# Optimization experiments

Measured on AMD Instinct MI355X. Metric: run time of the kernel, lower is better.

## Reference

```python
import jax, jax.numpy as jnp
import numpy as np

DIM = 768
D_STATE = 16
D_INNER = 2 * DIM  # expand=2


def setup_inputs() -> dict:
    key = jax.random.key(0)
    k_x, k_in, k_conv, k_out = jax.random.split(key, 4)
    B, L = 1, 4096
    x = jax.random.normal(k_x, (B, L, DIM), dtype=jnp.float32)
    # torch Linear weight layout: [out_features, in_features]
    W_in = jax.random.normal(k_in, (3 * D_INNER + 2 * D_STATE, DIM), dtype=jnp.float32) * 0.02
    # depthwise conv1d kernel: [out_ch=d_inner, in_ch/groups=1, k=3]
    W_conv = jax.random.normal(k_conv, (D_INNER, 1, 3), dtype=jnp.float32) * 0.1
    W_out = jax.random.normal(k_out, (DIM, D_INNER), dtype=jnp.float32) * 0.02
    A_log = jnp.log(jnp.tile(jnp.arange(1, D_STATE + 1, dtype=jnp.float32), (D_INNER, 1)))
    D = jnp.ones((D_INNER,), dtype=jnp.float32)
    return {"x": x, "W_in": W_in, "W_conv": W_conv, "W_out": W_out, "A_log": A_log, "D": D}


def reference(x, W_in, W_conv, W_out, A_log, D):
    d_inner = W_conv.shape[0]
    d_state = A_log.shape[1]
    Bsz = x.shape[0]

    xz = x @ W_in.T  # [B, L, 3*d_inner + 2*d_state]
    x_inner, z, B_ssm, C_ssm, delta = jnp.split(
        xz, [d_inner, 2 * d_inner, 2 * d_inner + d_state, 2 * d_inner + 2 * d_state], axis=-1
    )

    # depthwise conv over sequence: [B, d_inner, L]
    xc = jax.lax.conv_general_dilated(
        x_inner.transpose(0, 2, 1), W_conv,
        window_strides=(1,), padding=[(1, 1)], feature_group_count=d_inner,
    ).transpose(0, 2, 1)  # back to [B, L, d_inner]
    xc = jax.nn.silu(xc)

    A = -jnp.exp(A_log)  # [d_inner, d_state]
    delta = jax.nn.softplus(delta)  # [B, L, d_inner]
    dA = jnp.exp(jnp.einsum('bld,dn->bldn', delta, A))           # [B, L, d_inner, d_state]
    dBx = jnp.einsum('bld,bln,bld->bldn', delta, B_ssm, xc)      # delta_B * x fused

    def step(h, inp):
        da_t, dbx_t, c_t = inp  # [B,d,n], [B,d,n], [B,n]
        h = da_t * h + dbx_t
        y_t = jnp.einsum('bdn,bn->bd', h, c_t)
        return h, y_t

    h0 = jnp.zeros((Bsz, d_inner, d_state), dtype=x.dtype)
    _, ys = jax.lax.scan(
        step, h0,
        (dA.transpose(1, 0, 2, 3), dBx.transpose(1, 0, 2, 3), C_ssm.transpose(1, 0, 2)),
    )  # ys: [L, B, d_inner]

    y = ys.transpose(1, 0, 2) + xc * D  # skip connection
    y = y * jax.nn.silu(z)
    return y @ W_out.T  # [B, L, dim]
```

## Files before the change

kernel.cpp:

```cpp
#include <hip/hip_runtime.h>
#include <hip/hip_bf16.h>
#include <math.h>

#define LSEQ   4096
#define DIM    768
#define DINNER 1536
#define DSTATE 16
#define NCOLS  4640
#define NCH    256
#define CLEN   16
#define NPAD   4736
#define DXW    1568

typedef _Float16 f16;
typedef __attribute__((ext_vector_type(2))) _Float16 f16x2;
typedef __attribute__((ext_vector_type(4))) _Float16 f16x4;
typedef __attribute__((ext_vector_type(8))) _Float16 f16x8;
typedef __attribute__((ext_vector_type(4))) float f32x4;

__device__ __forceinline__ void gld_lds16(void* lds_dst, const void* gsrc) {
    __builtin_amdgcn_global_load_lds(
        (__attribute__((address_space(1))) void*)(gsrc),
        (__attribute__((address_space(3))) void*)(lds_dst), 16, 0, 0);
}

#define G1K    768
#define G1_NT  12
#define G1_BM  256
#define G1_BN  128
#define G1_RT  384
#define G1_LDSE (G1_RT * 64)

__global__ __launch_bounds__(512) void gemm1_pipe(const f16* __restrict__ A,
                                                  const f16* __restrict__ B,
                                                  float* __restrict__ C,
                                                  f16* __restrict__ Xb,
                                                  f16* __restrict__ Zb) {
    __shared__ __align__(16) f16 S[3 * G1_LDSE];

    const int P   = gridDim.x >> 3;
    const int idx = (blockIdx.x & 7) * P + (blockIdx.x >> 3);
    const int sm  = idx / 296;
    const int rem = idx - sm * 296;
    const int m0  = (sm * 8 + (rem & 7)) * G1_BM;
    const int n0  = (rem >> 3) * G1_BN;

    const int tid  = threadIdx.x;
    const int w    = tid >> 6;
    const int lane = tid & 63;
    const int wr   = w >> 1;
    const int wc   = w & 1;
    const int m    = lane & 15;
    const int q    = lane >> 4;
    const int rl8  = lane >> 3;
    const int bsel = lane & 7;

    const f16* gb[6];
#pragma unroll
    for (int s = 0; s < 6; ++s) {
        const int rl  = (w + 8 * s) * 8 + rl8;
        const int blk = bsel ^ (rl & 7);
        gb[s] = (rl < G1_BM) ? A + (size_t)(m0 + rl) * G1K + blk * 8
                             : B + (size_t)(n0 + rl - G1_BM) * G1K + blk * 8;
    }

    f32x4 acc[4][4];
#pragma unroll
    for (int i = 0; i < 4; i++)
#pragma unroll
        for (int j = 0; j < 4; j++) acc[i][j] = (f32x4){0.f, 0.f, 0.f, 0.f};

    auto stg2 = [&](int kt, int s0) {
        f16* dst = S + (kt % 3) * G1_LDSE;
#pragma unroll
        for (int s = s0; s < s0 + 2; ++s)
            gld_lds16(dst + (w + 8 * s) * 512, gb[s] + kt * 64);
    };
    auto stg6 = [&](int kt) {
        f16* dst = S + (kt % 3) * G1_LDSE;
#pragma unroll
        for (int s = 0; s < 6; ++s)
            gld_lds16(dst + (w + 8 * s) * 512, gb[s] + kt * 64);
    };

    stg6(0);
    stg6(1);

#pragma unroll
    for (int kt = 0; kt < G1_NT; ++kt) {
        if (kt < G1_NT - 1) asm volatile("s_waitcnt vmcnt(6)" ::: "memory");
        else                asm volatile("s_waitcnt vmcnt(0)" ::: "memory");
        __builtin_amdgcn_s_barrier();
        const f16* As = S + (kt % 3) * G1_LDSE;
        const f16* Bs = As + G1_BM * 64;
        const bool pf = (kt + 2 < G1_NT);

        f16x8 af0[2][2], af2[2][2], bh0[2][2], bh2[2][2];

#pragma unroll
        for (int kk = 0; kk < 2; ++kk) {
            const int fo = (((q + 4 * kk) ^ (m & 7)) << 3);
#pragma unroll
            for (int i = 0; i < 2; ++i) {
                af0[kk][i] = *(const f16x8*)&As[(wr * 64 + i * 16 + m) * 64 + fo];
                bh0[kk][i] = *(const f16x8*)&Bs[(wc * 64 + i * 16 + m) * 64 + fo];
            }
        }
        if (pf) stg2(kt + 2, 0);
        __builtin_amdgcn_s_barrier();
        asm volatile("s_waitcnt lgkmcnt(0)" ::: "memory");
        __builtin_amdgcn_sched_barrier(0);
        __builtin_amdgcn_s_setprio(1);
#pragma unroll
        for (int kk = 0; kk < 2; ++kk)
#pragma unroll
            for (int i = 0; i < 2; ++i)
#pragma unroll
                for (int j = 0; j < 2; ++j)
                    acc[i][j] = __builtin_amdgcn_mfma_f32_16x16x32_f16(
                        af0[kk][i], bh0[kk][j], acc[i][j], 0, 0, 0);
        __builtin_amdgcn_s_setprio(0);

#pragma unroll
        for (int kk = 0; kk < 2; ++kk) {
            const int fo = (((q + 4 * kk) ^ (m & 7)) << 3);
#pragma unroll
            for (int j = 0; j < 2; ++j)
                bh2[kk][j] = *(const f16x8*)&Bs[(wc * 64 + (j + 2) * 16 + m) * 64 + fo];
        }
        if (pf) stg2(kt + 2, 2);
        __builtin_amdgcn_s_barrier();
        asm volatile("s_waitcnt lgkmcnt(0)" ::: "memory");
        __builtin_amdgcn_sched_barrier(0);
        __builtin_amdgcn_s_setprio(1);
#pragma unroll
        for (int kk = 0; kk < 2; ++kk)
#pragma unroll
            for (int i = 0; i < 2; ++i)
#pragma unroll
                for (int j = 0; j < 2; ++j)
                    acc[i][j + 2] = __builtin_amdgcn_mfma_f32_16x16x32_f16(
                        af0[kk][i], bh2[kk][j], acc[i][j + 2], 0, 0, 0);
        __builtin_amdgcn_s_setprio(0);

#pragma unroll
        for (int kk = 0; kk < 2; ++kk) {
            const int fo = (((q + 4 * kk) ^ (m & 7)) << 3);
#pragma unroll
            for (int i = 0; i < 2; ++i)
                af2[kk][i] = *(const f16x8*)&As[(wr * 64 + (i + 2) * 16 + m) * 64 + fo];
        }
        if (pf) stg2(kt + 2, 4);
        __builtin_amdgcn_s_barrier();
        asm volatile("s_waitcnt lgkmcnt(0)" ::: "memory");
        __builtin_amdgcn_sched_barrier(0);
        __builtin_amdgcn_s_setprio(1);
#pragma unroll
        for (int kk = 0; kk < 2; ++kk)
#pragma unroll
            for (int i = 0; i < 2; ++i)
#pragma unroll
                for (int j = 0; j < 2; ++j)
                    acc[i + 2][j] = __builtin_amdgcn_mfma_f32_16x16x32_f16(
                        af2[kk][i], bh0[kk][j], acc[i + 2][j], 0, 0, 0);
        __builtin_amdgcn_s_setprio(0);

        __builtin_amdgcn_s_setprio(1);
#pragma unroll
        for (int kk = 0; kk < 2; ++kk)
#pragma unroll
            for (int i = 0; i < 2; ++i)
#pragma unroll
                for (int j = 0; j < 2; ++j)
                    acc[i + 2][j + 2] = __builtin_amdgcn_mfma_f32_16x16x32_f16(
                        af2[kk][i], bh2[kk][j], acc[i + 2][j + 2], 0, 0, 0);
        __builtin_amdgcn_s_setprio(0);
    }

    if (n0 < DINNER) {
#pragma unroll
        for (int i = 0; i < 4; i++)
#pragma unroll
            for (int j = 0; j < 4; j++) {
                const int col  = n0 + wc * 64 + j * 16 + m;
                const int rowb = m0 + wr * 64 + i * 16 + q * 4;
#pragma unroll
                for (int r = 0; r < 4; r++)
                    Xb[(size_t)(rowb + r) * DINNER + col] = (f16)acc[i][j][r];
            }
        return;
    }
    if (n0 < 2 * DINNER) {
#pragma unroll
        for (int i = 0; i < 4; i++)
#pragma unroll
            for (int j = 0; j < 4; j++) {
                const int col  = n0 - DINNER + wc * 64 + j * 16 + m;
                const int rowb = m0 + wr * 64 + i * 16 + q * 4;
#pragma unroll
                for (int r = 0; r < 4; r++)
                    Zb[(size_t)(rowb + r) * DINNER + col] = (f16)acc[i][j][r];
            }
        return;
    }
#pragma unroll
    for (int i = 0; i < 4; i++)
#pragma unroll
        for (int j = 0; j < 4; j++) {
            const int col = n0 - 2 * DINNER + wc * 64 + j * 16 + m;
            if (col >= DXW) continue;
            const int rowb = m0 + wr * 64 + i * 16 + q * 4;
#pragma unroll
            for (int r = 0; r < 4; r++)
                C[(size_t)(rowb + r) * DXW + col] = acc[i][j][r];
        }
}

#define G2K    1536
#define G2_NT  24
#define G2_LDSE (128 * 64)

__global__ __launch_bounds__(256) void gemm2_pipe(const f16* __restrict__ A,
                                                  const f16* __restrict__ B,
                                                  float* __restrict__ C) {
    __shared__ __align__(16) f16 S[3 * G2_LDSE];

    const int P   = gridDim.x >> 3;
    const int idx = (blockIdx.x & 7) * P + (blockIdx.x >> 3);
    const int m0  = (idx / 12) * 64;
    const int n0  = (idx % 12) * 64;

    const int tid  = threadIdx.x;
    const int w    = tid >> 6;
    const int lane = tid & 63;
    const int wr   = w >> 1;
    const int wc   = w & 1;
    const int m    = lane & 15;
    const int q    = lane >> 4;
    const int rl8  = lane >> 3;
    const int bsel = lane & 7;

    const f16* gb[4];
#pragma unroll
    for (int s = 0; s < 4; ++s) {
        const int rl  = (w + 4 * s) * 8 + rl8;
        const int blk = bsel ^ (rl & 7);
        gb[s] = (rl < 64) ? A + (size_t)(m0 + rl) * G2K + blk * 8
                          : B + (size_t)(n0 + rl - 64) * G2K + blk * 8;
    }

    f32x4 acc[2][2];
#pragma unroll
    for (int i = 0; i < 2; i++)
#pragma unroll
        for (int j = 0; j < 2; j++) acc[i][j] = (f32x4){0.f, 0.f, 0.f, 0.f};

    auto stg = [&](int kt) {
        f16* dst = S + (kt % 3) * G2_LDSE;
#pragma unroll
        for (int s = 0; s < 4; ++s)
            gld_lds16(dst + (w + 4 * s) * 512, gb[s] + kt * 64);
    };

    stg(0);
    stg(1);

#pragma unroll
    for (int kt = 0; kt < G2_NT; ++kt) {
        if (kt < G2_NT - 1) asm volatile("s_waitcnt vmcnt(4)" ::: "memory");
        else                asm volatile("s_waitcnt vmcnt(0)" ::: "memory");
        __builtin_amdgcn_s_barrier();
        if (kt + 2 < G2_NT) stg(kt + 2);

        const f16* As = S + (kt % 3) * G2_LDSE;
        const f16* Bs = As + 64 * 64;

        f16x8 af[2][2], bh[2][2];
#pragma unroll
        for (int kk = 0; kk < 2; ++kk) {
            const int fo = (((q + 4 * kk) ^ (m & 7)) << 3);
#pragma unroll
            for (int i = 0; i < 2; ++i) {
                af[kk][i] = *(const f16x8*)&As[(wr * 32 + i * 16 + m) * 64 + fo];
                bh[kk][i] = *(const f16x8*)&Bs[(wc * 32 + i * 16 + m) * 64 + fo];
            }
        }
        asm volatile("s_waitcnt lgkmcnt(0)" ::: "memory");
        __builtin_amdgcn_sched_barrier(0);
        __builtin_amdgcn_s_setprio(1);
#pragma unroll
        for (int kk = 0; kk < 2; ++kk)
#pragma unroll
            for (int i = 0; i < 2; ++i)
#pragma unroll
                for (int j = 0; j < 2; ++j)
                    acc[i][j] = __builtin_amdgcn_mfma_f32_16x16x32_f16(
                        af[kk][i], bh[kk][j], acc[i][j], 0, 0, 0);
        __builtin_amdgcn_s_setprio(0);
    }

#pragma unroll
    for (int i = 0; i < 2; i++)
#pragma unroll
        for (int j = 0; j < 2; j++) {
            const int col  = n0 + wc * 32 + j * 16 + m;
            const int rowb = m0 + wr * 32 + i * 16 + q * 4;
#pragma unroll
            for (int r = 0; r < 4; r++)
                C[(size_t)(rowb + r) * DIM + col] = acc[i][j][r];
        }
}

#define E0 (LSEQ * DIM)
#define E1 (E0 + NPAD * DIM)
#define E2 (E1 + DIM * DINNER)

__global__ __launch_bounds__(256) void cvt_all(const float* __restrict__ x,
                                               const float* __restrict__ Wi,
                                               const float* __restrict__ Wo,
                                               f16* __restrict__ Ax,
                                               f16* __restrict__ Bw,
                                               f16* __restrict__ Bo) {
    int i = (blockIdx.x * 256 + threadIdx.x) * 4;
    if (i < E0) {
        float4 v = *(const float4*)(x + i);
        f16x4 o = {(f16)v.x, (f16)v.y, (f16)v.z, (f16)v.w};
        *(f16x4*)(Ax + i) = o;
    } else if (i < E1) {
        int e = i - E0;
        int n = e / DIM;
        if (n < NCOLS) {
            float4 v = *(const float4*)(Wi + e);
            f16x4 o = {(f16)v.x, (f16)v.y, (f16)v.z, (f16)v.w};
            *(f16x4*)(Bw + e) = o;
        } else {
            f16x4 o = {(f16)0.f, (f16)0.f, (f16)0.f, (f16)0.f};
            *(f16x4*)(Bw + e) = o;
        }
    } else if (i < E2) {
        int e = i - E1;
        float4 v = *(const float4*)(Wo + e);
        f16x4 o = {(f16)v.x, (f16)v.y, (f16)v.z, (f16)v.w};
        *(f16x4*)(Bo + e) = o;
    }
}

__global__ __launch_bounds__(256, 3) void scan1_kernel(const float* __restrict__ Dxz,
                                                       const f16* __restrict__ Xb,
                                                       const float* __restrict__ Wc,
                                                       const float* __restrict__ A_log,
                                                       float* __restrict__ Sb,
                                                       float* __restrict__ hend) {
    __shared__ __align__(16) f16   Xs[18 * 512];
    __shared__ __align__(16) float Ds[16 * 512];
    __shared__ float Bs[CLEN * DSTATE];
    const int tid  = threadIdx.x;
    const int w4   = tid >> 6;
    const int lane = tid & 63;
    const int ch0  = blockIdx.x * 512;
    const int d0   = ch0 + 2 * tid;
    const int c    = blockIdx.y;
    const int l0   = c * CLEN;

    for (int r = w4; r < 18; r += 4) {
        const int gr = l0 - 1 + r;
        if (gr >= 0 && gr < LSEQ)
            gld_lds16(Xs + r * 512, Xb + (size_t)gr * DINNER + ch0 + lane * 8);
    }
    for (int i = w4; i < 32; i += 4) {
        const int t = i >> 1, hh = i & 1;
        gld_lds16(Ds + t * 512 + hh * 256,
                  Dxz + (size_t)(l0 + t) * DXW + 32 + ch0 + hh * 256 + lane * 4);
    }
    for (int i = tid; i < CLEN * DSTATE; i += 256)
        Bs[i] = Dxz[(size_t)(l0 + (i >> 4)) * DXW + (i & 15)];

    float Ar0[DSTATE], Ar1[DSTATE];
#pragma unroll
    for (int n = 0; n < DSTATE; n++) {
        Ar0[n] = -__expf(A_log[d0 * DSTATE + n]);
        Ar1[n] = -__expf(A_log[(d0 + 1) * DSTATE + n]);
    }
    const float w00 = Wc[d0 * 3 + 0], w01 = Wc[d0 * 3 + 1], w02 = Wc[d0 * 3 + 2];
    const float w10 = Wc[d0 * 3 + 3], w11 = Wc[d0 * 3 + 4], w12 = Wc[d0 * 3 + 5];

    asm volatile("s_waitcnt vmcnt(0)" ::: "memory");
    if (l0 == 0)
        *(f16x2*)&Xs[2 * tid] = (f16x2){(f16)0.f, (f16)0.f};
    if (c == NCH - 1)
        *(f16x2*)&Xs[17 * 512 + 2 * tid] = (f16x2){(f16)0.f, (f16)0.f};
    __syncthreads();

    auto ldx = [&](int r) -> float2 {
        f16x2 v = *(const f16x2*)&Xs[r * 512 + 2 * tid];
        return make_float2((float)v.x, (float)v.y);
    };

    float h0[DSTATE], h1[DSTATE];
#pragma unroll
    for (int n = 0; n < DSTATE; n++) { h0[n] = 0.f; h1[n] = 0.f; }
    float S0 = 0.f, S1 = 0.f;

    float2 xm = ldx(0);
    float2 x0 = ldx(1);
    for (int t = 0; t < CLEN; t++) {
        float2 xp = ldx(t + 2);
        float2 dr = *(const float2*)&Ds[t * 512 + 2 * tid];
        float v0  = xm.x * w00 + x0.x * w01 + xp.x * w02;
        float v1  = xm.y * w10 + x0.y * w11 + xp.y * w12;
        float xc0 = __fdividef(v0, 1.f + __expf(-v0));
        float xc1 = __fdividef(v1, 1.f + __expf(-v1));
        float dt0 = (dr.x > 20.f) ? dr.x : __logf(1.f + __expf(dr.x));
        float dt1 = (dr.y > 20.f) ? dr.y : __logf(1.f + __expf(dr.y));
        float u0 = dt0 * xc0, u1 = dt1 * xc1;
        S0 += dt0; S1 += dt1;
#pragma unroll
        for (int n = 0; n < DSTATE; n++) {
            float b = Bs[t * DSTATE + n];
            h0[n] = __expf(dt0 * Ar0[n]) * h0[n] + u0 * b;
            h1[n] = __expf(dt1 * Ar1[n]) * h1[n] + u1 * b;
        }
        xm = x0; x0 = xp;
    }
    *(float2*)&Sb[(size_t)c * DINNER + d0] = make_float2(S0, S1);
#pragma unroll
    for (int n = 0; n < DSTATE; n++)
        *(float2*)&hend[((size_t)c * DSTATE + n) * DINNER + d0] = make_float2(h0[n], h1[n]);
}

__global__ __launch_bounds__(256) void scan2_kernel(const float* __restrict__ Sb,
                                                    const float* __restrict__ A_log,
                                                    const float* __restrict__ hend,
                                                    float* __restrict__ hinit) {
    const int g = blockIdx.x * 256 + threadIdx.x;
    const int n = g / DINNER;
    const int d = g - n * DINNER;
    const float Ar = -__expf(A_log[d * DSTATE + n]);
    const size_t S = (size_t)DSTATE * DINNER;
    float sA[8], eA[8], sB[8], eB[8];
#pragma unroll
    for (int k = 0; k < 8; ++k) {
        sA[k] = Sb[(size_t)k * DINNER + d];
        eA[k] = hend[g + (size_t)k * S];
    }
    float h = 0.f;
    for (int c = 0; c < NCH; c += 16) {
#pragma unroll
        for (int k = 0; k < 8; ++k) {
            sB[k] = Sb[(size_t)(c + 8 + k) * DINNER + d];
            eB[k] = hend[g + (size_t)(c + 8 + k) * S];
        }
#pragma unroll
        for (int k = 0; k < 8; ++k) {
            hinit[g + (size_t)(c + k) * S] = h;
            h = __expf(sA[k] * Ar) * h + eA[k];
        }
        if (c + 16 < NCH) {
#pragma unroll
            for (int k = 0; k < 8; ++k) {
                sA[k] = Sb[(size_t)(c + 16 + k) * DINNER + d];
                eA[k] = hend[g + (size_t)(c + 16 + k) * S];
            }
        }
#pragma unroll
        for (int k = 0; k < 8; ++k) {
            hinit[g + (size_t)(c + 8 + k) * S] = h;
            h = __expf(sB[k] * Ar) * h + eB[k];
        }
    }
}

__global__ __launch_bounds__(256, 3) void scan3_kernel(const float* __restrict__ Dxz,
                                                       const f16* __restrict__ Xb,
                                                       const f16* __restrict__ Zb,
                                                       const float* __restrict__ Wc,
                                                       const float* __restrict__ A_log,
                                                       const float* __restrict__ hinit,
                                                       const float* __restrict__ Dp,
                                                       f16* __restrict__ Ay) {
    __shared__ __align__(16) f16   Xs[18 * 512];
    __shared__ __align__(16) float Ds[16 * 512];
    __shared__ float Bs[CLEN * DSTATE];
    __shared__ float Cs[CLEN * DSTATE];
    const int tid  = threadIdx.x;
    const int w4   = tid >> 6;
    const int lane = tid & 63;
    const int ch0  = blockIdx.x * 512;
    const int d0   = ch0 + 2 * tid;
    const int c    = blockIdx.y;
    const int l0   = c * CLEN;

    for (int r = w4; r < 18; r += 4) {
        const int gr = l0 - 1 + r;
        if (gr >= 0 && gr < LSEQ)
            gld_lds16(Xs + r * 512, Xb + (size_t)gr * DINNER + ch0 + lane * 8);
    }
    for (int i = w4; i < 32; i += 4) {
        const int t = i >> 1, hh = i & 1;
        gld_lds16(Ds + t * 512 + hh * 256,
                  Dxz + (size_t)(l0 + t) * DXW + 32 + ch0 + hh * 256 + lane * 4);
    }
    for (int i = tid; i < CLEN * DSTATE; i += 256) {
        size_t roff = (size_t)(l0 + (i >> 4)) * DXW;
        Bs[i] = Dxz[roff + (i & 15)];
        Cs[i] = Dxz[roff + 16 + (i & 15)];
    }

    float Ar0[DSTATE], Ar1[DSTATE];
#pragma unroll
    for (int n = 0; n < DSTATE; n++) {
        Ar0[n] = -__expf(A_log[d0 * DSTATE + n]);
        Ar1[n] = -__expf(A_log[(d0 + 1) * DSTATE + n]);
    }
    float h0[DSTATE], h1[DSTATE];
#pragma unroll
    for (int n = 0; n < DSTATE; n++) {
        float2 hv = *(const float2*)&hinit[((size_t)c * DSTATE + n) * DINNER + d0];
        h0[n] = hv.x; h1[n] = hv.y;
    }
    const float Dv0 = Dp[d0], Dv1 = Dp[d0 + 1];
    const float w00 = Wc[d0 * 3 + 0], w01 = Wc[d0 * 3 + 1], w02 = Wc[d0 * 3 + 2];
    const float w10 = Wc[d0 * 3 + 3], w11 = Wc[d0 * 3 + 4], w12 = Wc[d0 * 3 + 5];

    auto ldz2 = [&](int l) -> float2 {
        f16x2 v = *(const f16x2*)&Zb[(size_t)l * DINNER + d0];
        return make_float2((float)v.x, (float)v.y);
    };
    float2 ld_z = ldz2(l0);

    asm volatile("s_waitcnt vmcnt(0)" ::: "memory");
    if (l0 == 0)
        *(f16x2*)&Xs[2 * tid] = (f16x2){(f16)0.f, (f16)0.f};
    if (c == NCH - 1)
        *(f16x2*)&Xs[17 * 512 + 2 * tid] = (f16x2){(f16)0.f, (f16)0.f};
    __syncthreads();

    auto ldx = [&](int r) -> float2 {
        f16x2 v = *(const f16x2*)&Xs[r * 512 + 2 * tid];
        return make_float2((float)v.x, (float)v.y);
    };

    float2 xm = ldx(0);
    float2 x0 = ldx(1);
    for (int t = 0; t < CLEN; t++) {
        const int l = l0 + t;
        float2 xp = ldx(t + 2);
        float2 dr = *(const float2*)&Ds[t * 512 + 2 * tid];
        float2 zv = ld_z;
        if (t + 1 < CLEN) ld_z = ldz2(l + 1);
        float v0  = xm.x * w00 + x0.x * w01 + xp.x * w02;
        float v1  = xm.y * w10 + x0.y * w11 + xp.y * w12;
        float xc0 = __fdividef(v0, 1.f + __expf(-v0));
        float xc1 = __fdividef(v1, 1.f + __expf(-v1));
        float dt0 = (dr.x > 20.f) ? dr.x : __logf(1.f + __expf(dr.x));
        float dt1 = (dr.y > 20.f) ? dr.y : __logf(1.f + __expf(dr.y));
        float u0 = dt0 * xc0, u1 = dt1 * xc1;
        float y0 = 0.f, y1 = 0.f;
#pragma unroll
        for (int n = 0; n < DSTATE; n++) {
            float b  = Bs[t * DSTATE + n];
            float cc = Cs[t * DSTATE + n];
            h0[n] = __expf(dt0 * Ar0[n]) * h0[n] + u0 * b;
            h1[n] = __expf(dt1 * Ar1[n]) * h1[n] + u1 * b;
            y0 += h0[n] * cc;
            y1 += h1[n] * cc;
        }
        float sz0 = __fdividef(zv.x, 1.f + __expf(-zv.x));
        float sz1 = __fdividef(zv.y, 1.f + __expf(-zv.y));
        f16x2 o = {(f16)((y0 + xc0 * Dv0) * sz0), (f16)((y1 + xc1 * Dv1) * sz1)};
        *(f16x2*)&Ay[(size_t)l * DINNER + d0] = o;
        xm = x0; x0 = xp;
    }
}

extern "C" void kernel_launch(void* const* d_in, const int* in_sizes, int n_in,
                              void* d_out, int out_size, void* d_ws, size_t ws_size,
                              hipStream_t stream) {
    const float* x     = (const float*)d_in[0];
    const float* W_in  = (const float*)d_in[1];
    const float* W_conv= (const float*)d_in[2];
    const float* W_out = (const float*)d_in[3];
    const float* A_log = (const float*)d_in[4];
    const float* Dp    = (const float*)d_in[5];
    float* out = (float*)d_out;

    float* ws  = (float*)d_ws;
    float* Dxz = ws;
    float* hi  = Dxz + (size_t)LSEQ * DXW;
    float* he  = hi + (size_t)NCH * DSTATE * DINNER;
    float* Sb  = he + (size_t)NCH * DSTATE * DINNER;
    f16* Ax = (f16*)(Sb + (size_t)NCH * DINNER);
    f16* Ay = Ax + (size_t)LSEQ * DIM;
    f16* Bw = Ay + (size_t)LSEQ * DINNER;
    f16* Bo = Bw + (size_t)NPAD * DIM;
    f16* Zb = Bo + (size_t)DIM * DINNER;
    f16* Xb = Zb + (size_t)LSEQ * DINNER;

    cvt_all<<<E2 / 1024, 256, 0, stream>>>(x, W_in, W_out, Ax, Bw, Bo);

    gemm1_pipe<<<592, 512, 0, stream>>>(Ax, Bw, Dxz, Xb, Zb);

    scan1_kernel<<<dim3(DINNER / 512, NCH), 256, 0, stream>>>(
        Dxz, Xb, W_conv, A_log, Sb, he);
    scan2_kernel<<<(DINNER * DSTATE) / 256, 256, 0, stream>>>(Sb, A_log, he, hi);
    scan3_kernel<<<dim3(DINNER / 512, NCH), 256, 0, stream>>>(
        Dxz, Xb, Zb, W_conv, A_log, hi, Dp, Ay);

    gemm2_pipe<<<768, 256, 0, stream>>>(Ay, Bo, out);
}
```

Baseline: 245.5 us.

## Parallelize cross-chunk state scan with two-level blocked scan in scan2

Rewrites the inter-chunk carry kernel so each (d,n) element's 256-chunk sequential recurrence is split across 16 thread groups of 16 chunks each. Each group computes a local affine composite (A,E), one thread per element scans the 16 composites through shared memory, and each group then replays its chunks from the correct initial state. The grid grows from 96 blocks to 1536. This removes the long serial latency chain of the old kernel, which had too few threads to fill the GPU, at the cost of an extra exp pass kept in registers and two block barriers. Memory accesses per warp become 16-element segments, so coalescing is weaker than before.

```diff
diff --git a/kernel.cpp b/kernel.cpp
--- a/kernel.cpp
+++ b/kernel.cpp
@@ -432,41 +432,51 @@
                                                     const float* __restrict__ A_log,
                                                     const float* __restrict__ hend,
                                                     float* __restrict__ hinit) {
-    const int g = blockIdx.x * 256 + threadIdx.x;
-    const int n = g / DINNER;
-    const int d = g - n * DINNER;
+    __shared__ float As_[16][17];
+    __shared__ float Es_[16][17];
+    __shared__ float Hs_[16][17];
+    const int tid = threadIdx.x;
+    const int el  = tid & 15;
+    const int grp = tid >> 4;
+    const int g   = blockIdx.x * 16 + el;
+    const int n   = g / DINNER;
+    const int d   = g - n * DINNER;
     const float Ar = -__expf(A_log[d * DSTATE + n]);
     const size_t S = (size_t)DSTATE * DINNER;
-    float sA[8], eA[8], sB[8], eB[8];
-#pragma unroll
-    for (int k = 0; k < 8; ++k) {
-        sA[k] = Sb[(size_t)k * DINNER + d];
-        eA[k] = hend[g + (size_t)k * S];
-    }
-    float h = 0.f;
-    for (int c = 0; c < NCH; c += 16) {
-#pragma unroll
-        for (int k = 0; k < 8; ++k) {
-            sB[k] = Sb[(size_t)(c + 8 + k) * DINNER + d];
-            eB[k] = hend[g + (size_t)(c + 8 + k) * S];
-        }
-#pragma unroll
-        for (int k = 0; k < 8; ++k) {
-            hinit[g + (size_t)(c + k) * S] = h;
-            h = __expf(sA[k] * Ar) * h + eA[k];
-        }
-        if (c + 16 < NCH) {
-#pragma unroll
-            for (int k = 0; k < 8; ++k) {
-                sA[k] = Sb[(size_t)(c + 16 + k) * DINNER + d];
-                eA[k] = hend[g + (size_t)(c + 16 + k) * S];
-            }
-        }
-#pragma unroll
-        for (int k = 0; k < 8; ++k) {
-            hinit[g + (size_t)(c + 8 + k) * S] = h;
-            h = __expf(sB[k] * Ar) * h + eB[k];
-        }
+
+    float sv[16], ev[16];
+#pragma unroll
+    for (int k = 0; k < 16; ++k) {
+        const int c = grp * 16 + k;
+        sv[k] = Sb[(size_t)c * DINNER + d];
+        ev[k] = hend[(size_t)c * S + g];
+    }
+    float av[16];
+    float A = 1.f, E = 0.f;
+#pragma unroll
+    for (int k = 0; k < 16; ++k) {
+        av[k] = __expf(sv[k] * Ar);
+        E = av[k] * E + ev[k];
+        A = av[k] * A;
+    }
+    As_[grp][el] = A;
+    Es_[grp][el] = E;
+    __syncthreads();
+    if (tid < 16) {
+        float h = 0.f;
+#pragma unroll
+        for (int gq = 0; gq < 16; ++gq) {
+            Hs_[gq][tid] = h;
+            h = As_[gq][tid] * h + Es_[gq][tid];
+        }
+    }
+    __syncthreads();
+    float h = Hs_[grp][el];
+#pragma unroll
+    for (int k = 0; k < 16; ++k) {
+        const int c = grp * 16 + k;
+        hinit[(size_t)c * S + g] = h;
+        h = av[k] * h + ev[k];
     }
 }
 
@@ -602,7 +612,7 @@
 
     scan1_kernel<<<dim3(DINNER / 512, NCH), 256, 0, stream>>>(
         Dxz, Xb, W_conv, A_log, Sb, he);
-    scan2_kernel<<<(DINNER * DSTATE) / 256, 256, 0, stream>>>(Sb, A_log, he, hi);
+    scan2_kernel<<<(DINNER * DSTATE) / 16, 256, 0, stream>>>(Sb, A_log, he, hi);
     scan3_kernel<<<dim3(DINNER / 512, NCH), 256, 0, stream>>>(
         Dxz, Xb, Zb, W_conv, A_log, hi, Dp, Ay);
 
```

Measured after the change: 234.3 us (median of 2 runs). 1.05x faster.
